# Optimization experiments

Measured on AMD Instinct MI355X. Metric: run time of the kernel, lower is better.

The kernel has to match this reference:

```python
import jax, jax.numpy as jnp
import numpy as np

B, T, D = 4, 2048, 768
H = 12
DH = D // H
DFF = 3072
EPS = 1e-5


def _layernorm(x, g, b):
    mu = jnp.mean(x, axis=-1, keepdims=True)
    var = jnp.var(x, axis=-1, keepdims=True)
    return (x - mu) * jax.lax.rsqrt(var + EPS) * g + b


def setup_inputs() -> dict:
    key = jax.random.key(0)
    ks = jax.random.split(key, 12)
    s = lambda fan_in: 1.0 / np.sqrt(fan_in)
    return {
        "x": jax.random.normal(ks[0], (B, T, D), dtype=jnp.float32),
        "ln1_g": jnp.ones((D,), jnp.float32),
        "ln1_b": jnp.zeros((D,), jnp.float32),
        "w_qkv": jax.random.uniform(ks[1], (D, 3 * D), jnp.float32, -s(D), s(D)),
        "b_qkv": jax.random.uniform(ks[2], (3 * D,), jnp.float32, -s(D), s(D)),
        "w_proj": jax.random.uniform(ks[3], (D, D), jnp.float32, -s(D), s(D)),
        "b_proj": jax.random.uniform(ks[4], (D,), jnp.float32, -s(D), s(D)),
        "ln2_g": jnp.ones((D,), jnp.float32),
        "ln2_b": jnp.zeros((D,), jnp.float32),
        "w_ff1": jax.random.uniform(ks[5], (D, DFF), jnp.float32, -s(D), s(D)),
        "b_ff1": jax.random.uniform(ks[6], (DFF,), jnp.float32, -s(D), s(D)),
        "w_ff2": jax.random.uniform(ks[7], (DFF, D), jnp.float32, -s(DFF), s(DFF)),
        "b_ff2": jax.random.uniform(ks[8], (D,), jnp.float32, -s(DFF), s(DFF)),
    }


def reference(x, ln1_g, ln1_b, w_qkv, b_qkv, w_proj, b_proj,
              ln2_g, ln2_b, w_ff1, b_ff1, w_ff2, b_ff2):
    # --- attention sublayer ---
    h = _layernorm(x, ln1_g, ln1_b)
    qkv = h @ w_qkv + b_qkv                       # [B,T,3D]
    q, k, v = jnp.split(qkv, 3, axis=-1)
    q = q.reshape(B, T, H, DH).transpose(0, 2, 1, 3)  # [B,H,T,DH]
    k = k.reshape(B, T, H, DH).transpose(0, 2, 1, 3)
    v = v.reshape(B, T, H, DH).transpose(0, 2, 1, 3)
    att = jnp.einsum('bhqd,bhkd->bhqk', q, k) / jnp.sqrt(jnp.float32(DH))
    causal = jnp.tril(jnp.ones((T, T), dtype=bool))
    att = jnp.where(causal, att, -jnp.inf)
    att = jax.nn.softmax(att, axis=-1)
    out = jnp.einsum('bhqk,bhkd->bhqd', att, v)    # [B,H,T,DH]
    out = out.transpose(0, 2, 1, 3).reshape(B, T, D)
    x = x + out @ w_proj + b_proj
    # --- MLP sublayer ---
    h2 = _layernorm(x, ln2_g, ln2_b)
    h2 = jax.nn.gelu(h2 @ w_ff1 + b_ff1, approximate=False)
    x = x + h2 @ w_ff2 + b_ff2
    return x
```

## Files before the change

kernel.cpp:

```cpp
#include <hip/hip_runtime.h>
#include <cstdint>
#include <cstddef>

typedef unsigned short u16;
typedef unsigned int u32;
typedef __attribute__((ext_vector_type(8))) short s16x8;
typedef __attribute__((ext_vector_type(4))) float f32x4;

#define NB 4
#define NT 2048
#define ND 768
#define NH 12
#define NDH 64
#define NFF 3072
#define NM (NB*NT)

__device__ __forceinline__ u16 f2b(float f){
  union { float f; unsigned u; } c; c.f = f;
  unsigned r = c.u + 0x7fffu + ((c.u >> 16) & 1u);
  return (u16)(r >> 16);
}

__device__ __forceinline__ f32x4 mfma16(s16x8 a, s16x8 b, f32x4 c){
  return __builtin_amdgcn_mfma_f32_16x16x32_bf16(a, b, c, 0, 0, 0);
}

__device__ __forceinline__ void stage16(u16* lds, const u16* g){
  __builtin_amdgcn_global_load_lds(
      (const __attribute__((address_space(1))) unsigned int*)g,
      (__attribute__((address_space(3))) unsigned int*)lds,
      16, 0, 0);
}

__device__ __forceinline__ float gelu_f(float v){
  const float x = v * 0.70710678118654752f;
  const float ax = fabsf(x);
  const float t = 1.f / (1.f + 0.3275911f * ax);
  const float y = t * (0.254829592f + t * (-0.284496736f + t * (1.421413741f
                + t * (-1.453152027f + t * 1.061405429f))));
  float er = 1.f - y * __expf(-ax * ax);
  er = copysignf(er, x);
  return 0.5f * v * (1.f + er);
}

__global__ __launch_bounds__(256) void pre_kernel(
    const float* __restrict__ w_qkv, const float* __restrict__ w_proj,
    const float* __restrict__ w_ff1, const float* __restrict__ w_ff2,
    u16* __restrict__ o_qkv, u16* __restrict__ o_proj,
    u16* __restrict__ o_ff1, u16* __restrict__ o_ff2,
    const float* __restrict__ x, const float* __restrict__ ln_g,
    const float* __restrict__ ln_b, u16* __restrict__ ln_out)
{
  const int t = threadIdx.x;
  if (blockIdx.x >= 6912) {
    const int row = blockIdx.x - 6912;
    const float* xr = x + (size_t)row * ND;
    float v0 = xr[t], v1 = xr[t + 256], v2 = xr[t + 512];
    float s = v0 + v1 + v2;
    float ss = v0*v0 + v1*v1 + v2*v2;
    #pragma unroll
    for (int o = 32; o; o >>= 1) { s += __shfl_xor(s, o, 64); ss += __shfl_xor(ss, o, 64); }
    __shared__ float red[8];
    const int w = t >> 6;
    if ((t & 63) == 0) { red[w] = s; red[4 + w] = ss; }
    __syncthreads();
    s  = red[0] + red[1] + red[2] + red[3];
    ss = red[4] + red[5] + red[6] + red[7];
    const float mu = s * (1.f / ND);
    const float var = ss * (1.f / ND) - mu * mu;
    const float rinv = rsqrtf(var + 1e-5f);
    u16* orow = ln_out + (size_t)row * ND;
    orow[t]       = f2b((v0 - mu) * rinv * ln_g[t]       + ln_b[t]);
    orow[t + 256] = f2b((v1 - mu) * rinv * ln_g[t + 256] + ln_b[t + 256]);
    orow[t + 512] = f2b((v2 - mu) * rinv * ln_g[t + 512] + ln_b[t + 512]);
    return;
  }
  int bid = blockIdx.x;
  const float* in; u16* out; int K, N, nx;
  if (bid < 1728)      { in = w_qkv;  out = o_qkv;  K = 768;  N = 2304; nx = 72; }
  else if ((bid -= 1728) < 576)  { in = w_proj; out = o_proj; K = 768;  N = 768;  nx = 24; }
  else if ((bid -= 576) < 2304)  { in = w_ff1;  out = o_ff1;  K = 768;  N = 3072; nx = 96; }
  else { bid -= 2304;              in = w_ff2;  out = o_ff2;  K = 3072; N = 768;  nx = 24; }
  const int n0 = (bid % nx) * 32, k0 = (bid / nx) * 32;

  __shared__ float tile[32][33];
  const int tx = t & 31, ty = t >> 5;
  #pragma unroll
  for (int i = 0; i < 32; i += 8)
    tile[ty + i][tx] = in[(size_t)(k0 + ty + i) * N + n0 + tx];
  __syncthreads();
  #pragma unroll
  for (int i = 0; i < 32; i += 8)
    out[(size_t)(n0 + ty + i) * K + k0 + tx] = f2b(tile[tx][ty + i]);
}

__global__ __launch_bounds__(256) void ln_kernel(
    const float* __restrict__ x, const float* __restrict__ g,
    const float* __restrict__ b, u16* __restrict__ out)
{
  const int row = blockIdx.x;
  const int t = threadIdx.x;
  const float* xr = x + (size_t)row * ND;
  float v0 = xr[t], v1 = xr[t + 256], v2 = xr[t + 512];
  float s = v0 + v1 + v2;
  float ss = v0*v0 + v1*v1 + v2*v2;
  #pragma unroll
  for (int o = 32; o; o >>= 1) { s += __shfl_xor(s, o, 64); ss += __shfl_xor(ss, o, 64); }
  __shared__ float red[8];
  const int w = t >> 6;
  if ((t & 63) == 0) { red[w] = s; red[4 + w] = ss; }
  __syncthreads();
  s  = red[0] + red[1] + red[2] + red[3];
  ss = red[4] + red[5] + red[6] + red[7];
  const float mu = s * (1.f / ND);
  const float var = ss * (1.f / ND) - mu * mu;
  const float rinv = rsqrtf(var + 1e-5f);
  u16* orow = out + (size_t)row * ND;
  orow[t]       = f2b((v0 - mu) * rinv * g[t]       + b[t]);
  orow[t + 256] = f2b((v1 - mu) * rinv * g[t + 256] + b[t + 256]);
  orow[t + 512] = f2b((v2 - mu) * rinv * g[t + 512] + b[t + 512]);
}

template<int EPI, int BM>
__global__ __launch_bounds__(256, (BM == 128) ? 3 : 4) void gemm_bt(
    const u16* __restrict__ A, const u16* __restrict__ Bt,
    const float* __restrict__ bias, const float* __restrict__ res,
    void* __restrict__ o0, void* __restrict__ o1, void* __restrict__ o2,
    const int M, const int N, const int K)
{
  constexpr int MI = BM / 64;
  __shared__ u16 As[3][BM * 32];
  __shared__ u16 Bs[3][128 * 32];
  const int tid = threadIdx.x;
  const int lane = tid & 63, wid = tid >> 6;
  const int wr = wid >> 1, wc = wid & 1;
  const int lg = lane >> 4, lm = lane & 15;
  const int bm = blockIdx.x * BM, bn = blockIdx.y * 128;

  f32x4 acc[2 * MI][4] = {};

  const int srow = tid >> 2;
  const int schunk = (tid & 3) ^ ((tid >> 3) & 3);
  const u16* ApT = A  + (size_t)(bm + srow) * K + schunk * 8;
  const u16* BpT = Bt + (size_t)(bn + srow) * K + schunk * 8;
  const size_t rs64 = (size_t)64 * K;
  const int woff = wid * 512;
  const int fswz = (lm >> 1) & 3;

  const int nt = K >> 5;

  #pragma unroll
  for (int p = 0; p < 2; ++p) {
    const int k0 = p << 5;
    stage16(&As[p][woff], ApT + k0);
    if (BM == 128) stage16(&As[p][woff + 2048], ApT + rs64 + k0);
    stage16(&Bs[p][woff],        BpT + k0);
    stage16(&Bs[p][woff + 2048], BpT + rs64 + k0);
  }

  for (int t = 0; t < nt; ++t) {
    if (t < nt - 1) {
      if (BM == 128) asm volatile("s_waitcnt vmcnt(4)" ::: "memory");
      else           asm volatile("s_waitcnt vmcnt(3)" ::: "memory");
    } else {
      asm volatile("s_waitcnt vmcnt(0)" ::: "memory");
    }
    __builtin_amdgcn_s_barrier();
    __builtin_amdgcn_sched_barrier(0);
    if (t + 2 < nt) {
      const int k0 = (t + 2) << 5;
      const int wb = (t + 2) % 3;
      stage16(&As[wb][woff], ApT + k0);
      if (BM == 128) stage16(&As[wb][woff + 2048], ApT + rs64 + k0);
      stage16(&Bs[wb][woff],        BpT + k0);
      stage16(&Bs[wb][woff + 2048], BpT + rs64 + k0);
    }
    __builtin_amdgcn_sched_barrier(0);
    const int rb = t % 3;
    s16x8 af[2 * MI], bf[4];
    #pragma unroll
    for (int i = 0; i < 2 * MI; i++)
      af[i] = *(const s16x8*)&As[rb][(wr * (BM / 2) + i * 16 + lm) * 32 + ((lg ^ fswz) * 8)];
    #pragma unroll
    for (int j = 0; j < 4; j++)
      bf[j] = *(const s16x8*)&Bs[rb][(wc * 64 + j * 16 + lm) * 32 + ((lg ^ fswz) * 8)];
    #pragma unroll
    for (int i = 0; i < 2 * MI; i++)
      #pragma unroll
      for (int j = 0; j < 4; j++)
        acc[i][j] = mfma16(af[i], bf[j], acc[i][j]);
  }

  #pragma unroll
  for (int i = 0; i < 2 * MI; i++)
    #pragma unroll
    for (int j = 0; j < 4; j++) {
      const int col = bn + wc * 64 + j * 16 + lm;
      const float bb = bias[col];
      #pragma unroll
      for (int r = 0; r < 4; r++) {
        const int row = bm + wr * (BM / 2) + i * 16 + lg * 4 + r;
        float v = acc[i][j][r] + bb;
        if (EPI == 0) {
          u16* dst; int rem;
          if (col < ND)            { dst = (u16*)o0; rem = col; v *= 0.125f; }
          else if (col < 2 * ND)   { dst = (u16*)o1; rem = col - ND; }
          else                     { dst = (u16*)o2; rem = col - 2 * ND; }
          const int hh = rem >> 6, dh = rem & 63;
          const int bb2 = row >> 11, tt = row & 2047;
          dst[(((size_t)bb2 * NH + hh) * NT + tt) * NDH + dh] = f2b(v);
        } else if (EPI == 1) {
          ((float*)o0)[(size_t)row * ND + col] = v + res[(size_t)row * ND + col];
        } else if (EPI == 2) {
          ((u16*)o0)[(size_t)row * NFF + col] = f2b(gelu_f(v));
        } else {
          ((float*)o0)[(size_t)row * ND + col] = v + res[(size_t)row * ND + col];
        }
      }
    }
}

__global__ __launch_bounds__(256,3) void attn_kernel(
    const u16* __restrict__ Q, const u16* __restrict__ Kg,
    const u16* __restrict__ V, u16* __restrict__ O)
{
  const int p  = blockIdx.y;
  const int bh = blockIdx.x;
  const int b = bh / NH, h = bh % NH;
  const int tid = threadIdx.x;
  const int lane = tid & 63, w = tid >> 6;
  const int lg = lane >> 4, lm = lane & 15;
  const int sr = tid >> 3;
  const int sc = (tid & 7) * 8;

  __shared__ u16 Ks[64 * 64];
  __shared__ u16 Vt[64 * 64];
  __shared__ u16 Ps[4][16 * 64];

  const u16* Qb = Q  + (size_t)bh * NT * NDH;
  const u16* Kb = Kg + (size_t)bh * NT * NDH;
  const u16* Vb = V  + (size_t)bh * NT * NDH;

  const int si0 = p, si1 = 31 - p;
  const int q00 = si0 * 64, q01 = si1 * 64;
  const int ktmax = si1;

  const s16x8 q0a = *(const s16x8*)&Qb[(size_t)(q00 + w * 16 + lm) * NDH + lg * 8];
  const s16x8 q0b = *(const s16x8*)&Qb[(size_t)(q00 + w * 16 + lm) * NDH + 32 + lg * 8];
  const s16x8 q1a = *(const s16x8*)&Qb[(size_t)(q01 + w * 16 + lm) * NDH + lg * 8];
  const s16x8 q1b = *(const s16x8*)&Qb[(size_t)(q01 + w * 16 + lm) * NDH + 32 + lg * 8];

  f32x4 oacc0[4] = {}, oacc1[4] = {};
  float m0 = -INFINITY, l0 = 0.f, m1 = -INFINITY, l1 = 0.f;

  auto do_strip = [&](const s16x8& qa, const s16x8& qb, f32x4* oacc,
                      float& m, float& l, bool diag) {
    f32x4 sv[4];
    #pragma unroll
    for (int n = 0; n < 4; ++n) {
      const int krow = (n * 16 + lm) * 64;
      const int swz = (lm & 7) << 3;
      s16x8 kf0 = *(const s16x8*)&Ks[krow + ((lg * 8) ^ swz)];
      s16x8 kf1 = *(const s16x8*)&Ks[krow + ((32 + lg * 8) ^ swz)];
      f32x4 s4 = {};
      s4 = mfma16(kf0, qa, s4);
      s4 = mfma16(kf1, qb, s4);
      sv[n] = s4;
    }
    if (diag) {
      #pragma unroll
      for (int n = 0; n < 4; ++n)
        #pragma unroll
        for (int r = 0; r < 4; ++r)
          if (n * 16 + lg * 4 + r > w * 16 + lm) sv[n][r] = -INFINITY;
    }
    float mx = -INFINITY;
    #pragma unroll
    for (int n = 0; n < 4; ++n)
      #pragma unroll
      for (int r = 0; r < 4; ++r) mx = fmaxf(mx, sv[n][r]);
    mx = fmaxf(mx, __shfl_xor(mx, 16));
    mx = fmaxf(mx, __shfl_xor(mx, 32));

    const bool defer = __all(mx - m <= 8.f);
    float alpha = 1.f;
    if (!defer) {
      const float mnew = fmaxf(m, mx);
      alpha = __expf(m - mnew);
      m = mnew;
    }

    float rs = 0.f;
    u32 pk[4][2];
    #pragma unroll
    for (int n = 0; n < 4; ++n) {
      const float p0 = __expf(sv[n][0] - m);
      const float p1 = __expf(sv[n][1] - m);
      const float p2 = __expf(sv[n][2] - m);
      const float p3 = __expf(sv[n][3] - m);
      rs += (p0 + p1) + (p2 + p3);
      pk[n][0] = (u32)f2b(p0) | ((u32)f2b(p1) << 16);
      pk[n][1] = (u32)f2b(p2) | ((u32)f2b(p3) << 16);
    }
    rs += __shfl_xor(rs, 16);
    rs += __shfl_xor(rs, 32);

    #pragma unroll
    for (int n = 0; n < 4; ++n) {
      const int idx0 = lm * 64 + ((n * 16 + lg * 4) ^ ((lm & 7) << 3));
      *(u32*)&Ps[w][idx0] = pk[n][0];
      *(u32*)&Ps[w][idx0 + 2] = pk[n][1];
    }

    if (!defer) {
      l = l * alpha + rs;
      float av[4];
      #pragma unroll
      for (int r = 0; r < 4; ++r) av[r] = __shfl(alpha, lg * 4 + r);
      #pragma unroll
      for (int d = 0; d < 4; ++d)
        #pragma unroll
        for (int r = 0; r < 4; ++r) oacc[d][r] *= av[r];
    } else {
      l += rs;
    }

    #pragma unroll
    for (int kh = 0; kh < 2; ++kh) {
      const s16x8 pf = *(const s16x8*)&Ps[w][lm * 64 + ((kh * 32 + lg * 8) ^ ((lm & 7) << 3))];
      #pragma unroll
      for (int dt = 0; dt < 4; ++dt) {
        const int g = ((2 * dt + (lm >> 3)) ^ (lm & 7)) & 7;
        const s16x8 vf = *(const s16x8*)&Vt[(dt * 16 + lm) * 64 + (((kh * 4 + lg) ^ g) << 3)];
        oacc[dt] = mfma16(pf, vf, oacc[dt]);
      }
    }
  };

  s16x8 kva = *(const s16x8*)&Kb[(size_t)sr * NDH + sc];
  s16x8 kvb = *(const s16x8*)&Kb[(size_t)(sr + 32) * NDH + sc];
  s16x8 vva = *(const s16x8*)&Vb[(size_t)sr * NDH + sc];
  s16x8 vvb = *(const s16x8*)&Vb[(size_t)(sr + 32) * NDH + sc];

  for (int kt = 0; kt <= ktmax; ++kt) {
    __syncthreads();
    *(s16x8*)&Ks[sr * 64 + (sc ^ ((sr & 7) << 3))] = kva;
    *(s16x8*)&Ks[(sr + 32) * 64 + (sc ^ ((sr & 7) << 3))] = kvb;
    #pragma unroll
    for (int e = 0; e < 8; ++e)
      Vt[(sc + e) * 64 + (sr ^ ((((tid & 7) ^ e)) << 3))] = (u16)vva[e];
    #pragma unroll
    for (int e = 0; e < 8; ++e)
      Vt[(sc + e) * 64 + ((sr + 32) ^ ((((tid & 7) ^ e)) << 3))] = (u16)vvb[e];
    __syncthreads();

    if (kt < ktmax) {
      const u16* Kn = Kb + (size_t)(kt + 1) * 64 * NDH;
      const u16* Vn = Vb + (size_t)(kt + 1) * 64 * NDH;
      kva = *(const s16x8*)&Kn[(size_t)sr * NDH + sc];
      kvb = *(const s16x8*)&Kn[(size_t)(sr + 32) * NDH + sc];
      vva = *(const s16x8*)&Vn[(size_t)sr * NDH + sc];
      vvb = *(const s16x8*)&Vn[(size_t)(sr + 32) * NDH + sc];
    }

    do_strip(q1a, q1b, oacc1, m1, l1, kt == si1);
    if (kt <= si0) do_strip(q0a, q0b, oacc0, m0, l0, kt == si0);
  }

  {
    float lv[4];
    #pragma unroll
    for (int r = 0; r < 4; ++r) lv[r] = 1.f / __shfl(l0, lg * 4 + r);
    #pragma unroll
    for (int dt = 0; dt < 4; ++dt)
      #pragma unroll
      for (int r = 0; r < 4; ++r) {
        const int qg = q00 + w * 16 + lg * 4 + r;
        O[((size_t)b * NT + qg) * ND + h * NDH + dt * 16 + lm] = f2b(oacc0[dt][r] * lv[r]);
      }
  }
  {
    float lv[4];
    #pragma unroll
    for (int r = 0; r < 4; ++r) lv[r] = 1.f / __shfl(l1, lg * 4 + r);
    #pragma unroll
    for (int dt = 0; dt < 4; ++dt)
      #pragma unroll
      for (int r = 0; r < 4; ++r) {
        const int qg = q01 + w * 16 + lg * 4 + r;
        O[((size_t)b * NT + qg) * ND + h * NDH + dt * 16 + lm] = f2b(oacc1[dt][r] * lv[r]);
      }
  }
}

extern "C" void kernel_launch(void* const* d_in, const int* in_sizes, int n_in,
                              void* d_out, int out_size, void* d_ws, size_t ws_size,
                              hipStream_t stream)
{
  const float* x      = (const float*)d_in[0];
  const float* ln1_g  = (const float*)d_in[1];
  const float* ln1_b  = (const float*)d_in[2];
  const float* w_qkv  = (const float*)d_in[3];
  const float* b_qkv  = (const float*)d_in[4];
  const float* w_proj = (const float*)d_in[5];
  const float* b_proj = (const float*)d_in[6];
  const float* ln2_g  = (const float*)d_in[7];
  const float* ln2_b  = (const float*)d_in[8];
  const float* w_ff1  = (const float*)d_in[9];
  const float* b_ff1  = (const float*)d_in[10];
  const float* w_ff2  = (const float*)d_in[11];
  const float* b_ff2  = (const float*)d_in[12];

  char* ws = (char*)d_ws;
  u16*   wt_qkv = (u16*)(ws + 0);
  u16*   wt_proj= (u16*)(ws + 3538944);
  u16*   wt_ff1 = (u16*)(ws + 4718592);
  u16*   wt_ff2 = (u16*)(ws + 9437184);
  u16*   hbuf   = (u16*)(ws + 14155776);
  u16*   qbuf   = (u16*)(ws + 26738688);
  u16*   kbuf   = (u16*)(ws + 39321600);
  u16*   vbuf   = (u16*)(ws + 51904512);
  u16*   aobuf  = (u16*)(ws + 64487424);
  float* x1     = (float*)(ws + 77070336);
  u16*   h2buf  = (u16*)(ws + 102236160);
  u16*   ff1buf = hbuf;

  pre_kernel<<<6912 + NM, 256, 0, stream>>>(w_qkv, w_proj, w_ff1, w_ff2,
                                            wt_qkv, wt_proj, wt_ff1, wt_ff2,
                                            x, ln1_g, ln1_b, hbuf);
  gemm_bt<0,128><<<dim3(NM/128, 2304/128), 256, 0, stream>>>(hbuf, wt_qkv, b_qkv, nullptr,
                                                             qbuf, kbuf, vbuf, NM, 2304, ND);
  attn_kernel<<<dim3(NB*NH, 16), 256, 0, stream>>>(qbuf, kbuf, vbuf, aobuf);
  gemm_bt<1,64><<<dim3(NM/64, ND/128), 256, 0, stream>>>(aobuf, wt_proj, b_proj, x,
                                                         x1, nullptr, nullptr, NM, ND, ND);
  ln_kernel<<<NM, 256, 0, stream>>>(x1, ln2_g, ln2_b, h2buf);
  gemm_bt<2,128><<<dim3(NM/128, NFF/128), 256, 0, stream>>>(h2buf, wt_ff1, b_ff1, nullptr,
                                                            ff1buf, nullptr, nullptr, NM, NFF, ND);
  gemm_bt<3,64><<<dim3(NM/64, ND/128), 256, 0, stream>>>(ff1buf, wt_ff2, b_ff2, x1,
                                                         d_out, nullptr, nullptr, NM, ND, NFF);
}
```

Baseline: 287.2 us.

## Add dedicated 128x256 triple-buffered GEMM kernel for FF1 with GELU epilogue

Replaces the generic 128x128 GEMM for the FF1 projection with a new 512-thread kernel computing 128x256 output tiles. It uses a three-stage shared-memory ring with swizzled LDS layout and explicit vmcnt waits, so loads run two k-steps ahead. The wider tile raises reuse of the A operand and the arithmetic per byte loaded. In exchange it uses more shared memory and more registers per block, and launches half as many blocks.

```diff
diff --git a/kernel.cpp b/kernel.cpp
--- a/kernel.cpp
+++ b/kernel.cpp
@@ -211,11 +211,84 @@
           dst[(((size_t)bb2 * NH + hh) * NT + tt) * NDH + dh] = f2b(v);
         } else if (EPI == 1) {
           ((float*)o0)[(size_t)row * ND + col] = v + res[(size_t)row * ND + col];
-        } else if (EPI == 2) {
-          ((u16*)o0)[(size_t)row * NFF + col] = f2b(gelu_f(v));
         } else {
           ((float*)o0)[(size_t)row * ND + col] = v + res[(size_t)row * ND + col];
         }
+      }
+    }
+}
+
+__global__ __launch_bounds__(512, 4) void gemm_wide(
+    const u16* __restrict__ A, const u16* __restrict__ Bt,
+    const float* __restrict__ bias, u16* __restrict__ o0,
+    const int K)
+{
+  __shared__ u16 As[3][128 * 32];
+  __shared__ u16 Bs[3][256 * 32];
+  const int tid = threadIdx.x;
+  const int lane = tid & 63, wid = tid >> 6;
+  const int wr = wid >> 2, wc = wid & 3;
+  const int lg = lane >> 4, lm = lane & 15;
+  const int bm = blockIdx.x * 128, bn = blockIdx.y * 256;
+
+  f32x4 acc[4][4] = {};
+
+  const int srow = tid >> 2;
+  const int schunk = (tid & 3) ^ ((tid >> 3) & 3);
+  const u16* ApT = A  + (size_t)(bm + srow) * K + schunk * 8;
+  const u16* BpT = Bt + (size_t)(bn + srow) * K + schunk * 8;
+  const size_t rs128 = (size_t)128 * K;
+  const int woff = wid * 512;
+  const int fswz = (lm >> 1) & 3;
+
+  const int nt = K >> 5;
+
+  #pragma unroll
+  for (int p = 0; p < 2; ++p) {
+    const int k0 = p << 5;
+    stage16(&As[p][woff],        ApT + k0);
+    stage16(&Bs[p][woff],        BpT + k0);
+    stage16(&Bs[p][woff + 4096], BpT + rs128 + k0);
+  }
+
+  for (int t = 0; t < nt; ++t) {
+    if (t < nt - 1) asm volatile("s_waitcnt vmcnt(3)" ::: "memory");
+    else            asm volatile("s_waitcnt vmcnt(0)" ::: "memory");
+    __builtin_amdgcn_s_barrier();
+    __builtin_amdgcn_sched_barrier(0);
+    if (t + 2 < nt) {
+      const int k0 = (t + 2) << 5;
+      const int wb = (t + 2) % 3;
+      stage16(&As[wb][woff],        ApT + k0);
+      stage16(&Bs[wb][woff],        BpT + k0);
+      stage16(&Bs[wb][woff + 4096], BpT + rs128 + k0);
+    }
+    __builtin_amdgcn_sched_barrier(0);
+    const int rb = t % 3;
+    s16x8 af[4], bf[4];
+    #pragma unroll
+    for (int i = 0; i < 4; i++)
+      af[i] = *(const s16x8*)&As[rb][(wr * 64 + i * 16 + lm) * 32 + ((lg ^ fswz) * 8)];
+    #pragma unroll
+    for (int j = 0; j < 4; j++)
+      bf[j] = *(const s16x8*)&Bs[rb][(wc * 64 + j * 16 + lm) * 32 + ((lg ^ fswz) * 8)];
+    #pragma unroll
+    for (int i = 0; i < 4; i++)
+      #pragma unroll
+      for (int j = 0; j < 4; j++)
+        acc[i][j] = mfma16(af[i], bf[j], acc[i][j]);
+  }
+
+  #pragma unroll
+  for (int i = 0; i < 4; i++)
+    #pragma unroll
+    for (int j = 0; j < 4; j++) {
+      const int col = bn + wc * 64 + j * 16 + lm;
+      const float bb = bias[col];
+      #pragma unroll
+      for (int r = 0; r < 4; r++) {
+        const int row = bm + wr * 64 + i * 16 + lg * 4 + r;
+        o0[(size_t)row * NFF + col] = f2b(gelu_f(acc[i][j][r] + bb));
       }
     }
 }
@@ -434,8 +507,7 @@
   gemm_bt<1,64><<<dim3(NM/64, ND/128), 256, 0, stream>>>(aobuf, wt_proj, b_proj, x,
                                                          x1, nullptr, nullptr, NM, ND, ND);
   ln_kernel<<<NM, 256, 0, stream>>>(x1, ln2_g, ln2_b, h2buf);
-  gemm_bt<2,128><<<dim3(NM/128, NFF/128), 256, 0, stream>>>(h2buf, wt_ff1, b_ff1, nullptr,
-                                                            ff1buf, nullptr, nullptr, NM, NFF, ND);
+  gemm_wide<<<dim3(NM/128, NFF/256), 512, 0, stream>>>(h2buf, wt_ff1, b_ff1, ff1buf, ND);
   gemm_bt<3,64><<<dim3(NM/64, ND/128), 256, 0, stream>>>(ff1buf, wt_ff2, b_ff2, x1,
                                                          d_out, nullptr, nullptr, NM, ND, NFF);
 }
```

New measurement: 287.1 us. About the same (-0.0%).
